# Kernel tuning notes

Measured on AMD Instinct MI355X. Metric: run time of the kernel, lower is better.

Reference implementation:

```python
import jax, jax.numpy as jnp
import numpy as np

K_ACT = 5          # k_active regimes
TAU = 0.5          # resample temperature
N = 8192           # n_particles (scaled to production size)
DZ, DM, KT, DE = 32, 64, 15, 16  # d_latent, d_mamba, k_regimes+10, d_regime_embed


def _lin(x, W, b):
    # torch nn.Linear convention: y = x @ W.T + b
    return x @ W.T + b


def setup_inputs() -> dict:
    key = jax.random.key(0)
    ks = iter(jax.random.split(key, 48))

    def rn(shape, s=1.0):
        return jax.random.normal(next(ks), shape, jnp.float32) * s

    inp = dict(
        remaining_high=jax.random.uniform(next(ks), (N,), jnp.float32) * 5.0 + 1.0,
        remaining_low=jax.random.uniform(next(ks), (N,), jnp.float32) * 5.0 + 1.0,
        z=rn((N, DZ)),
        regime_logits=rn((N, KT)),
        log_weights=rn((N,), 0.5),
        h_t=rn((DM,)),
        obs_remaining=jnp.float32(3.0),
        eps_high=rn((N,)),
        eps_low=rn((N,)),
        u_gumbel=jax.random.uniform(next(ks), (N, N), jnp.float32),
        embed=rn((KT, DE), 0.1),
        W_rt1=rn((32, DM + DE), 0.1), b_rt1=jnp.zeros(32, jnp.float32),
        W_rt2=rn((KT, 32), 0.1), b_rt2=jnp.zeros(KT, jnp.float32),
        W_d1=rn((64, DM + DE + DZ), 0.1), b_d1=jnp.zeros(64, jnp.float32),
        W_d2=rn((32, 64), 0.1), b_d2=jnp.zeros(32, jnp.float32),
        W_d3=rn((4, 32), 0.1), b_d3=jnp.zeros(4, jnp.float32),
        W_g=rn((DZ, DM + DE + DZ), 0.1), b_g=jnp.zeros(DZ, jnp.float32),
        W_c=rn((DZ, DM + DE + DZ), 0.1), b_c=jnp.zeros(DZ, jnp.float32),
        log_R=jnp.array([np.log(0.5), np.log(0.4), np.log(0.6)], jnp.float32),
        log_obs_scale=rn((KT,), 0.1),
        W_a1=rn((16, DM), 0.1), b_a1=jnp.zeros(16, jnp.float32),
        W_a2=rn((1, 16), 0.1), b_a2=jnp.zeros(1, jnp.float32),
    )
    return inp


def reference(remaining_high, remaining_low, z, regime_logits, log_weights, h_t,
              obs_remaining, eps_high, eps_low, u_gumbel, embed,
              W_rt1, b_rt1, W_rt2, b_rt2, W_d1, b_d1, W_d2, b_d2, W_d3, b_d3,
              W_g, b_g, W_c, b_c, log_R, log_obs_scale, W_a1, b_a1, W_a2, b_a2):
    silu = jax.nn.silu
    n = remaining_high.shape[0]
    h = jnp.broadcast_to(h_t, (n, h_t.shape[0]))  # (N, d_mamba)

    # ---- transition (predict step) ----
    rp = jax.nn.softmax(regime_logits, axis=-1)[:, :K_ACT]          # (N, K)
    remb = rp @ embed[:K_ACT]                                        # (N, d_embed)
    ri = jnp.concatenate([h, remb], axis=-1)                         # (N, 80)
    upd = _lin(silu(_lin(ri, W_rt1, b_rt1)), W_rt2, b_rt2)[:, :K_ACT]
    new_logits = regime_logits.at[:, :K_ACT].set(
        0.7 * regime_logits[:, :K_ACT] + 0.3 * upd)
    di = jnp.concatenate([h, remb, z], axis=-1)                      # (N, 112)
    dp = _lin(silu(_lin(silu(_lin(di, W_d1, b_d1)), W_d2, b_d2)), W_d3, b_d3)
    sig_h = jax.nn.softplus(dp[:, 2]) + 0.01
    sig_l = jax.nn.softplus(dp[:, 3]) + 0.01
    nh = jnp.clip(remaining_high + dp[:, 0] + sig_h * eps_high, 0.0)
    nl = jnp.clip(remaining_low + dp[:, 1] + sig_l * eps_low, 0.0)
    gate = jax.nn.sigmoid(_lin(di, W_g, b_g))
    nz = gate * z + (1.0 - gate) * jnp.tanh(_lin(di, W_c, b_c))

    # ---- observation: skew-normal log-likelihood (source_idx=0, 'high') ----
    R_src = jnp.clip(jnp.exp(log_R[0]), 0.15, 2.5)
    alpha = _lin(silu(_lin(h_t[None, :], W_a1, b_a1)), W_a2, b_a2)[0, 0]
    scales = jax.nn.softplus(log_obs_scale[:K_ACT])
    nrp = jax.nn.softmax(new_logits, axis=-1)[:, :K_ACT]
    R = jnp.clip(R_src * (nrp @ scales), 0.15, 4.0)                  # (N,)
    zz = (obs_remaining - nh) / R
    loglik = (jnp.log(2.0) - jnp.log(R) - 0.5 * jnp.log(2.0 * jnp.pi)
              - 0.5 * zz * zz + jax.scipy.stats.norm.logcdf(alpha * zz))

    # ---- weight update + normalization ----
    lw = log_weights + loglik
    lw = lw - jax.scipy.special.logsumexp(lw)

    # ---- soft resample (Gumbel-softmax relaxation) ----
    g = -jnp.log(-jnp.log(u_gumbel + 1e-10) + 1e-10)                 # (N, N)
    sa = jax.nn.softmax((lw[None, :] + g) / TAU, axis=-1)            # (N, N)
    state = jnp.concatenate([nh[:, None], nl[:, None], nz, new_logits], axis=-1)  # (N, 49)
    return sa @ state  # resampled [high | low | z | regime_logits]
```

## Files before the change

### kernel.cpp

```cpp
#include <hip/hip_runtime.h>
#include <math.h>

#define NP 8192

using f32x4  = __attribute__((ext_vector_type(4))) float;
using bf16x4 = __attribute__((ext_vector_type(4))) short;
using bf16x8 = __attribute__((ext_vector_type(8))) short;

__device__ __forceinline__ unsigned short f2bf(float x) {
  unsigned int u = __float_as_uint(x);
  u = (u + 0x7FFFu + ((u >> 16) & 1u)) >> 16;
  return (unsigned short)u;
}
__device__ __forceinline__ float fast_log2(float x) { float r; asm("v_log_f32 %0, %1" : "=v"(r) : "v"(x)); return r; }
__device__ __forceinline__ float fast_exp2(float x) { float r; asm("v_exp_f32 %0, %1" : "=v"(r) : "v"(x)); return r; }
__device__ __forceinline__ float siluf(float x) { return x / (1.0f + expf(-x)); }
__device__ __forceinline__ float softplusf(float x) { return (x > 20.0f) ? x : log1pf(expf(x)); }
__device__ __forceinline__ float dot4(const float4 a, const float4 b) {
  return a.x * b.x + a.y * b.y + a.z * b.z + a.w * b.w;
}


__global__ __launch_bounds__(128) void k_particle(
    const float* __restrict__ rh,   const float* __restrict__ rlo,
    const float* __restrict__ z,    const float* __restrict__ rlog,
    const float* __restrict__ logw, const float* __restrict__ h_t,
    const float* __restrict__ obs_p,
    const float* __restrict__ eps_h, const float* __restrict__ eps_l,
    const float* __restrict__ embed,
    const float* __restrict__ W_rt1, const float* __restrict__ b_rt1,
    const float* __restrict__ W_rt2, const float* __restrict__ b_rt2,
    const float* __restrict__ W_d1,  const float* __restrict__ b_d1,
    const float* __restrict__ W_d2,  const float* __restrict__ b_d2,
    const float* __restrict__ W_d3,  const float* __restrict__ b_d3,
    const float* __restrict__ W_g,   const float* __restrict__ b_g,
    const float* __restrict__ W_c,   const float* __restrict__ b_c,
    const float* __restrict__ log_R, const float* __restrict__ log_obs_scale,
    const float* __restrict__ W_a1,  const float* __restrict__ b_a1,
    const float* __restrict__ W_a2,  const float* __restrict__ b_a2,
    float* __restrict__ a_out, unsigned short* __restrict__ Bt) {
  __shared__ float d1c[64 * 48];
  __shared__ float gcs[32 * 48];
  __shared__ float ccs[32 * 48];
  __shared__ float rt1c[32 * 16];
  __shared__ float d2s[32 * 64];
  __shared__ float d3s[4 * 32];
  __shared__ float rt2s[5 * 32];
  __shared__ float embs[80];
  __shared__ float cD1[64], cRT1[32], cG[32], cC[32];
  __shared__ float bD2[32], bD3[4], bRT2[8];
  __shared__ float a1s[16], scal[8];
  __shared__ float x1ex[32 * 68];
  __shared__ float tx[32 * 36];
  __shared__ float stex[32 * 52];

  const int t = threadIdx.x;

#define STAGEM(DST, SRC, ROWS, SSTR, C0, NC)                          \
  for (int e = t; e < (ROWS) * (NC); e += 128) {                      \
    const int ro = e / (NC);                                          \
    const int co = e - ro * (NC);                                     \
    DST[e] = SRC[ro * (SSTR) + (C0) + co];                            \
  }
  STAGEM(d1c, W_d1, 64, 112, 64, 48)
  STAGEM(gcs, W_g, 32, 112, 64, 48)
  STAGEM(ccs, W_c, 32, 112, 64, 48)
  STAGEM(rt1c, W_rt1, 32, 80, 64, 16)
#undef STAGEM
  for (int e = t; e < 2048; e += 128) d2s[e] = W_d2[e];
  if (t < 128) d3s[t] = W_d3[t];
  for (int e = t; e < 160; e += 128) rt2s[e] = W_rt2[e];
  if (t < 80) embs[t] = embed[t];
  if (t < 32) bD2[t] = b_d2[t];
  if (t < 4)  bD3[t] = b_d3[t];
  if (t < 5)  bRT2[t] = b_rt2[t];

  for (int o = t; o < 160; o += 128) {
    const float* wr; float bb;
    if (o < 64)       { wr = W_d1 + o * 112;        bb = b_d1[o]; }
    else if (o < 96)  { wr = W_rt1 + (o - 64) * 80; bb = b_rt1[o - 64]; }
    else if (o < 128) { wr = W_g + (o - 96) * 112;  bb = b_g[o - 96]; }
    else              { wr = W_c + (o - 128) * 112; bb = b_c[o - 128]; }
    float acc = bb;
    #pragma unroll
    for (int m = 0; m < 64; m += 4)
      acc += dot4(*(const float4*)(wr + m), *(const float4*)(h_t + m));
    if (o < 64) cD1[o] = acc;
    else if (o < 96) cRT1[o - 64] = acc;
    else if (o < 128) cG[o - 96] = acc;
    else cC[o - 128] = acc;
  }
  if (t < 16) {
    float acc = b_a1[t];
    #pragma unroll
    for (int m = 0; m < 64; m += 4)
      acc += dot4(*(const float4*)(W_a1 + t * 64 + m), *(const float4*)(h_t + m));
    a1s[t] = siluf(acc);
  } else if (t == 16) {
    scal[1] = fminf(fmaxf(expf(log_R[0]), 0.15f), 2.5f);
  } else if (t >= 17 && t < 22) {
    scal[2 + t - 17] = softplusf(log_obs_scale[t - 17]);
  }
  __syncthreads();
  if (t == 0) {
    float acc = b_a2[0];
    #pragma unroll
    for (int k = 0; k < 16; ++k) acc += W_a2[k] * a1s[k];
    scal[0] = acc;
  }

  const int l = t & 63, lbase = l & ~3;
  const int q = t >> 2, s = t & 3;
  const int j = blockIdx.x * 32 + q;
  const float obs = obs_p[0];

  float rlj[15];
  #pragma unroll
  for (int k = 0; k < 15; ++k) rlj[k] = rlog[j * 15 + k];
  float m0 = rlj[0];
  #pragma unroll
  for (int k = 1; k < 15; ++k) m0 = fmaxf(m0, rlj[k]);
  float sum = 0.0f, e5[5];
  #pragma unroll
  for (int k = 0; k < 15; ++k) { float e = expf(rlj[k] - m0); if (k < 5) e5[k] = e; sum += e; }
  const float inv = 1.0f / sum;

  float remb[16];
  #pragma unroll
  for (int c = 0; c < 16; ++c) {
    float acc = e5[0] * embs[c];
    #pragma unroll
    for (int k = 1; k < 5; ++k) acc += e5[k] * embs[k * 16 + c];
    remb[c] = acc * inv;
  }

  float zj[32];
  #pragma unroll
  for (int c = 0; c < 32; c += 4) {
    const float4 v = *(const float4*)(z + j * 32 + c);
    zj[c] = v.x; zj[c + 1] = v.y; zj[c + 2] = v.z; zj[c + 3] = v.w;
  }

  #pragma unroll
  for (int r = 0; r < 8; ++r) {
    const int o = 4 * r + s;
    float acc = cRT1[o];
    #pragma unroll
    for (int c = 0; c < 16; ++c) acc += rt1c[o * 16 + c] * remb[c];
    tx[q * 36 + o] = siluf(acc);
  }
  __syncthreads();
  float t1[32];
  #pragma unroll
  for (int c = 0; c < 32; c += 4) {
    const float4 v = *(const float4*)(tx + q * 36 + c);
    t1[c] = v.x; t1[c + 1] = v.y; t1[c + 2] = v.z; t1[c + 3] = v.w;
  }
  float updS = bRT2[s], upd4 = bRT2[4];
  #pragma unroll
  for (int c = 0; c < 32; ++c) { updS += rt2s[s * 32 + c] * t1[c]; upd4 += rt2s[128 + c] * t1[c]; }
  float nlg[15];
  #pragma unroll
  for (int k = 0; k < 4; ++k) nlg[k] = 0.7f * rlj[k] + 0.3f * __shfl(updS, lbase + k);
  nlg[4] = 0.7f * rlj[4] + 0.3f * upd4;
  #pragma unroll
  for (int k = 5; k < 15; ++k) nlg[k] = rlj[k];

  #pragma unroll
  for (int r = 0; r < 16; ++r) {
    const int o = 4 * r + s;
    const float* wrow = d1c + o * 48;
    float acc = cD1[o];
    #pragma unroll
    for (int c = 0; c < 16; ++c) acc += wrow[c] * remb[c];
    #pragma unroll
    for (int c = 0; c < 32; ++c) acc += wrow[16 + c] * zj[c];
    x1ex[q * 68 + o] = siluf(acc);
  }
  __syncthreads();

  float acc8[8];
  #pragma unroll
  for (int r = 0; r < 8; ++r) acc8[r] = bD2[4 * r + s];
  #pragma unroll
  for (int half = 0; half < 2; ++half) {
    float xh[32];
    #pragma unroll
    for (int c = 0; c < 32; c += 4) {
      const float4 v = *(const float4*)(x1ex + q * 68 + half * 32 + c);
      xh[c] = v.x; xh[c + 1] = v.y; xh[c + 2] = v.z; xh[c + 3] = v.w;
    }
    #pragma unroll
    for (int r = 0; r < 8; ++r) {
      const int o = 4 * r + s;
      #pragma unroll
      for (int c = 0; c < 32; ++c) acc8[r] += d2s[o * 64 + half * 32 + c] * xh[c];
    }
  }
  #pragma unroll
  for (int r = 0; r < 8; ++r) tx[q * 36 + 4 * r + s] = siluf(acc8[r]);
  __syncthreads();
  float x2v[32];
  #pragma unroll
  for (int c = 0; c < 32; c += 4) {
    const float4 v = *(const float4*)(tx + q * 36 + c);
    x2v[c] = v.x; x2v[c + 1] = v.y; x2v[c + 2] = v.z; x2v[c + 3] = v.w;
  }
  float dps = bD3[s];
  #pragma unroll
  for (int c = 0; c < 32; ++c) dps += d3s[s * 32 + c] * x2v[c];
  const float dp0 = __shfl(dps, lbase), dp1 = __shfl(dps, lbase + 1);
  const float dp2 = __shfl(dps, lbase + 2), dp3 = __shfl(dps, lbase + 3);
  const float sig_h = softplusf(dp2) + 0.01f;
  const float sig_l = softplusf(dp3) + 0.01f;
  const float nh = fmaxf(rh[j] + dp0 + sig_h * eps_h[j], 0.0f);
  const float nl = fmaxf(rlo[j] + dp1 + sig_l * eps_l[j], 0.0f);

  #pragma unroll
  for (int r = 0; r < 8; ++r) {
    const int o = 4 * r + s;
    const float* gr = gcs + o * 48;
    const float* cr = ccs + o * 48;
    float ga = cG[o], caa = cC[o];
    #pragma unroll
    for (int c = 0; c < 16; ++c) { ga += gr[c] * remb[c]; caa += cr[c] * remb[c]; }
    #pragma unroll
    for (int c = 0; c < 32; ++c) { ga += gr[16 + c] * zj[c]; caa += cr[16 + c] * zj[c]; }
    const float gs = 1.0f / (1.0f + expf(-ga));
    stex[q * 52 + 2 + o] = gs * zj[o] + (1.0f - gs) * tanhf(caa);
  }

  if (s == 0) {
    stex[q * 52 + 0] = nh;
    stex[q * 52 + 1] = nl;
    #pragma unroll
    for (int k = 0; k < 15; ++k) stex[q * 52 + 34 + k] = nlg[k];
    float m1 = nlg[0];
    #pragma unroll
    for (int k = 1; k < 15; ++k) m1 = fmaxf(m1, nlg[k]);
    float sum1 = 0.0f, e5b[5];
    #pragma unroll
    for (int k = 0; k < 15; ++k) { float e = expf(nlg[k] - m1); if (k < 5) e5b[k] = e; sum1 += e; }
    float dot = 0.0f;
    #pragma unroll
    for (int k = 0; k < 5; ++k) dot += e5b[k] * scal[2 + k];
    dot /= sum1;
    const float R  = fminf(fmaxf(scal[1] * dot, 0.15f), 4.0f);
    const float zz = (obs - nh) / R;
    const float xx = scal[0] * zz;
    float lcdf;
    if (xx > -6.0f) {
      double p = 0.5 * erfc(-(double)xx * 0.7071067811865475244);
      lcdf = (float)log(p);
    } else {
      const float ix2 = 1.0f / (xx * xx);
      const float ser = 1.0f + ix2 * (-1.0f + ix2 * (3.0f + ix2 * (-15.0f + ix2 * 105.0f)));
      lcdf = -0.5f * xx * xx - logf(-xx) - 0.918938533f + logf(ser);
    }
    const float loglik = 0.693147181f - logf(R) - 0.918938533f - 0.5f * zz * zz + lcdf;
    a_out[j] = (logw[j] + loglik) * 2.8853900817779268f;
  }
  __syncthreads();

  if (t < 64) {
    const int c = t;
    const int b = c >> 4, rowc = c & 15;
    if (c < 49) {
      #pragma unroll
      for (int m = 0; m < 4; ++m) {
        bf16x8 v8;
        #pragma unroll
        for (int r = 0; r < 8; ++r) v8[r] = (short)f2bf(stex[(8 * m + r) * 52 + c]);
        *(bf16x8*)(Bt + (size_t)(((blockIdx.x * 4 + b) * 64) + m * 16 + rowc) * 8) = v8;
      }
    } else if (c == 49) {
      bf16x8 v8;
      #pragma unroll
      for (int r = 0; r < 8; ++r) v8[r] = (short)0x3F80;
      #pragma unroll
      for (int m = 0; m < 4; ++m)
        *(bf16x8*)(Bt + (size_t)(((blockIdx.x * 4 + b) * 64) + m * 16 + rowc) * 8) = v8;
    } else {
      bf16x8 v8;
      #pragma unroll
      for (int r = 0; r < 8; ++r) v8[r] = 0;
      #pragma unroll
      for (int m = 0; m < 4; ++m)
        *(bf16x8*)(Bt + (size_t)(((blockIdx.x * 4 + b) * 64) + m * 16 + rowc) * 8) = v8;
    }
  }
}

#define RSTR 136
__global__ __launch_bounds__(512) void k_resample(const float* __restrict__ u,
                                                  const float* __restrict__ a,
                                                  const unsigned short* __restrict__ Bt,
                                                  float* __restrict__ out) {
  __shared__ unsigned short Wlds[8][16][RSTR];
  __shared__ float cacc[8][64][16];
  __shared__ float zrow[16];
  const int t = threadIdx.x;
  const int w = t >> 6, l = t & 63;
  const int i0 = blockIdx.x << 4;
  const int jw = w << 10;
  const int lc = (l & 31) << 2;
  const int rh2 = l >> 5;

  f32x4 acc0 = {0.f, 0.f, 0.f, 0.f}, acc1 = acc0, acc2 = acc0, acc3 = acc0;

  for (int g = 0; g < 8; ++g) {
    const int cb = jw + (g << 7);
    const float4 av = *(const float4*)(a + cb + lc);
    float4 uv[8];
    #pragma unroll
    for (int q2 = 0; q2 < 8; ++q2) {
      const int row = (q2 << 1) + rh2;
      uv[q2] = *(const float4*)(u + (size_t)(i0 + row) * NP + cb + lc);
    }
    #pragma unroll
    for (int q2 = 0; q2 < 8; ++q2) {
      const int row = (q2 << 1) + rh2;
      bf16x4 wv4;
      #pragma unroll
      for (int e = 0; e < 4; ++e) {
        const float ue = (e == 0) ? uv[q2].x : (e == 1) ? uv[q2].y : (e == 2) ? uv[q2].z : uv[q2].w;
        const float ae = (e == 0) ? av.x : (e == 1) ? av.y : (e == 2) ? av.z : av.w;
        const float t1 = fast_log2(ue + 1e-10f);
        const float t2 = fmaf(t1, -0.69314718056f, 1e-10f);
        const float t3 = fast_log2(t2);
        wv4[e] = (short)f2bf(fast_exp2(fmaf(t3, -2.0f, ae)));
      }
      *(bf16x4*)(&Wlds[w][row][lc]) = wv4;
    }
    #pragma unroll
    for (int kbl = 0; kbl < 4; ++kbl) {
      const int jblk = (cb >> 5) + kbl;
      const bf16x8 af = *(const bf16x8*)(&Wlds[w][l & 15][(kbl << 5) + ((l >> 4) << 3)]);
      const unsigned short* bp = Bt + (size_t)(jblk << 2) * 512;
      const bf16x8 b0 = *(const bf16x8*)(bp + (0 * 64 + l) * 8);
      const bf16x8 b1 = *(const bf16x8*)(bp + (1 * 64 + l) * 8);
      const bf16x8 b2 = *(const bf16x8*)(bp + (2 * 64 + l) * 8);
      const bf16x8 b3 = *(const bf16x8*)(bp + (3 * 64 + l) * 8);
      acc0 = __builtin_amdgcn_mfma_f32_16x16x32_bf16(af, b0, acc0, 0, 0, 0);
      acc1 = __builtin_amdgcn_mfma_f32_16x16x32_bf16(af, b1, acc1, 0, 0, 0);
      acc2 = __builtin_amdgcn_mfma_f32_16x16x32_bf16(af, b2, acc2, 0, 0, 0);
      acc3 = __builtin_amdgcn_mfma_f32_16x16x32_bf16(af, b3, acc3, 0, 0, 0);
    }
  }

  __syncthreads();
  #pragma unroll
  for (int r = 0; r < 4; ++r) {
    cacc[w][l][0 * 4 + r] = acc0[r];
    cacc[w][l][1 * 4 + r] = acc1[r];
    cacc[w][l][2 * 4 + r] = acc2[r];
    cacc[w][l][3 * 4 + r] = acc3[r];
  }
  __syncthreads();

  const int c = t & 63;
  float v[2];
  #pragma unroll
  for (int rr = 0; rr < 2; ++rr) {
    const int r    = ((t >> 6) << 1) + rr;
    const int lsrc = ((r >> 2) << 4) | (c & 15);
    const int reg  = ((c >> 4) << 2) + (r & 3);
    float sv = 0.0f;
    #pragma unroll
    for (int ww = 0; ww < 8; ++ww) sv += cacc[ww][lsrc][reg];
    v[rr] = sv;
    if (c == 49) zrow[r] = sv;
  }
  __syncthreads();
  if (c < 49) {
    #pragma unroll
    for (int rr = 0; rr < 2; ++rr) {
      const int r = ((t >> 6) << 1) + rr;
      out[(size_t)(i0 + r) * 49 + c] = v[rr] / zrow[r];
    }
  }
}

extern "C" void kernel_launch(void* const* d_in, const int* in_sizes, int n_in,
                              void* d_out, int out_size, void* d_ws, size_t ws_size,
                              hipStream_t stream) {
  const float* rh    = (const float*)d_in[0];
  const float* rlo   = (const float*)d_in[1];
  const float* z     = (const float*)d_in[2];
  const float* rlog  = (const float*)d_in[3];
  const float* logw  = (const float*)d_in[4];
  const float* h_t   = (const float*)d_in[5];
  const float* obs   = (const float*)d_in[6];
  const float* eps_h = (const float*)d_in[7];
  const float* eps_l = (const float*)d_in[8];
  const float* u     = (const float*)d_in[9];
  const float* embed = (const float*)d_in[10];
  const float* W_rt1 = (const float*)d_in[11];
  const float* b_rt1 = (const float*)d_in[12];
  const float* W_rt2 = (const float*)d_in[13];
  const float* b_rt2 = (const float*)d_in[14];
  const float* W_d1  = (const float*)d_in[15];
  const float* b_d1  = (const float*)d_in[16];
  const float* W_d2  = (const float*)d_in[17];
  const float* b_d2  = (const float*)d_in[18];
  const float* W_d3  = (const float*)d_in[19];
  const float* b_d3  = (const float*)d_in[20];
  const float* W_g   = (const float*)d_in[21];
  const float* b_g   = (const float*)d_in[22];
  const float* W_c   = (const float*)d_in[23];
  const float* b_c   = (const float*)d_in[24];
  const float* log_R = (const float*)d_in[25];
  const float* log_obs_scale = (const float*)d_in[26];
  const float* W_a1  = (const float*)d_in[27];
  const float* b_a1  = (const float*)d_in[28];
  const float* W_a2  = (const float*)d_in[29];
  const float* b_a2  = (const float*)d_in[30];

  float* ws_a = (float*)((char*)d_ws + 36864);
  unsigned short* ws_bt = (unsigned short*)((char*)d_ws + 73728);

  k_particle<<<256, 128, 0, stream>>>(rh, rlo, z, rlog, logw, h_t, obs, eps_h, eps_l,
                                      embed, W_rt1, b_rt1, W_rt2, b_rt2,
                                      W_d1, b_d1, W_d2, b_d2, W_d3, b_d3,
                                      W_g, b_g, W_c, b_c, log_R, log_obs_scale,
                                      W_a1, b_a1, W_a2, b_a2, ws_a, ws_bt);
  k_resample<<<512, 512, 0, stream>>>(u, ws_a, ws_bt, (float*)d_out);
}
```

Measured before the change: 470.6 us.

## Double-buffer Gumbel tile loads, widen groups, and replace log/exp with reciprocal

The resample kernel now processes 256-column groups per wave and software-pipelines the global loads of the uniform noise tile: the next group's 16 rows are prefetched into registers while the current group is transformed and fed to MFMA. The Gumbel weight exp(a - 2*log(-log u)) is rewritten algebraically as exp2(a) * rcp(X)^2, replacing one log and one per-element exp with a reciprocal and hoisting exp2(a) out of the row loop. The LDS staging buffer and the cross-wave reduction buffer are aliased into one shared array. The cost is much higher register use from two 16-float4 tiles, which may lower occupancy or cause spills.

```diff
diff --git a/kernel.cpp b/kernel.cpp
--- a/kernel.cpp
+++ b/kernel.cpp
@@ -2,6 +2,7 @@
 #include <math.h>
 
 #define NP 8192
+#define RSTR 264
 
 using f32x4  = __attribute__((ext_vector_type(4))) float;
 using bf16x4 = __attribute__((ext_vector_type(4))) short;
@@ -14,6 +15,7 @@
 }
 __device__ __forceinline__ float fast_log2(float x) { float r; asm("v_log_f32 %0, %1" : "=v"(r) : "v"(x)); return r; }
 __device__ __forceinline__ float fast_exp2(float x) { float r; asm("v_exp_f32 %0, %1" : "=v"(r) : "v"(x)); return r; }
+__device__ __forceinline__ float fast_rcp(float x)  { float r; asm("v_rcp_f32 %0, %1" : "=v"(r) : "v"(x)); return r; }
 __device__ __forceinline__ float siluf(float x) { return x / (1.0f + expf(-x)); }
 __device__ __forceinline__ float softplusf(float x) { return (x > 20.0f) ? x : log1pf(expf(x)); }
 __device__ __forceinline__ float dot4(const float4 a, const float4 b) {
@@ -291,51 +293,81 @@
   }
 }
 
-#define RSTR 136
+struct UTile { float4 v[16]; };
+
+__device__ __forceinline__ void load_group(UTile& ut, float4& av,
+                                           const float* __restrict__ u,
+                                           const float* __restrict__ a,
+                                           int i0, int cb, int lc4) {
+  #pragma unroll
+  for (int r = 0; r < 16; ++r)
+    ut.v[r] = *(const float4*)(u + (size_t)(i0 + r) * NP + cb + lc4);
+  av = *(const float4*)(a + cb + lc4);
+}
+
+__device__ __forceinline__ void transform_store(const UTile& ut, const float4 av,
+                                                unsigned short* __restrict__ Wwave, int lc4) {
+  const float e2a0 = fast_exp2(av.x), e2a1 = fast_exp2(av.y);
+  const float e2a2 = fast_exp2(av.z), e2a3 = fast_exp2(av.w);
+  #pragma unroll
+  for (int r = 0; r < 16; ++r) {
+    bf16x4 o;
+    const float xs0 = ut.v[r].x, xs1 = ut.v[r].y, xs2 = ut.v[r].z, xs3 = ut.v[r].w;
+    {
+      const float X = fmaf(fast_log2(xs0 + 1e-10f), -0.69314718056f, 1e-10f);
+      const float rr = fast_rcp(X);
+      o[0] = (short)f2bf(e2a0 * rr * rr);
+    }
+    {
+      const float X = fmaf(fast_log2(xs1 + 1e-10f), -0.69314718056f, 1e-10f);
+      const float rr = fast_rcp(X);
+      o[1] = (short)f2bf(e2a1 * rr * rr);
+    }
+    {
+      const float X = fmaf(fast_log2(xs2 + 1e-10f), -0.69314718056f, 1e-10f);
+      const float rr = fast_rcp(X);
+      o[2] = (short)f2bf(e2a2 * rr * rr);
+    }
+    {
+      const float X = fmaf(fast_log2(xs3 + 1e-10f), -0.69314718056f, 1e-10f);
+      const float rr = fast_rcp(X);
+      o[3] = (short)f2bf(e2a3 * rr * rr);
+    }
+    *(bf16x4*)(Wwave + r * RSTR + lc4) = o;
+  }
+}
+
 __global__ __launch_bounds__(512) void k_resample(const float* __restrict__ u,
                                                   const float* __restrict__ a,
                                                   const unsigned short* __restrict__ Bt,
                                                   float* __restrict__ out) {
-  __shared__ unsigned short Wlds[8][16][RSTR];
-  __shared__ float cacc[8][64][16];
+  __shared__ __align__(16) char smem[8 * 16 * RSTR * 2];
   __shared__ float zrow[16];
   const int t = threadIdx.x;
   const int w = t >> 6, l = t & 63;
   const int i0 = blockIdx.x << 4;
   const int jw = w << 10;
-  const int lc = (l & 31) << 2;
-  const int rh2 = l >> 5;
+  const int lc4 = l << 2;
+  unsigned short* Wwave = (unsigned short*)smem + w * 16 * RSTR;
 
   f32x4 acc0 = {0.f, 0.f, 0.f, 0.f}, acc1 = acc0, acc2 = acc0, acc3 = acc0;
 
-  for (int g = 0; g < 8; ++g) {
-    const int cb = jw + (g << 7);
-    const float4 av = *(const float4*)(a + cb + lc);
-    float4 uv[8];
-    #pragma unroll
-    for (int q2 = 0; q2 < 8; ++q2) {
-      const int row = (q2 << 1) + rh2;
-      uv[q2] = *(const float4*)(u + (size_t)(i0 + row) * NP + cb + lc);
-    }
-    #pragma unroll
-    for (int q2 = 0; q2 < 8; ++q2) {
-      const int row = (q2 << 1) + rh2;
-      bf16x4 wv4;
-      #pragma unroll
-      for (int e = 0; e < 4; ++e) {
-        const float ue = (e == 0) ? uv[q2].x : (e == 1) ? uv[q2].y : (e == 2) ? uv[q2].z : uv[q2].w;
-        const float ae = (e == 0) ? av.x : (e == 1) ? av.y : (e == 2) ? av.z : av.w;
-        const float t1 = fast_log2(ue + 1e-10f);
-        const float t2 = fmaf(t1, -0.69314718056f, 1e-10f);
-        const float t3 = fast_log2(t2);
-        wv4[e] = (short)f2bf(fast_exp2(fmaf(t3, -2.0f, ae)));
-      }
-      *(bf16x4*)(&Wlds[w][row][lc]) = wv4;
-    }
-    #pragma unroll
-    for (int kbl = 0; kbl < 4; ++kbl) {
-      const int jblk = (cb >> 5) + kbl;
-      const bf16x8 af = *(const bf16x8*)(&Wlds[w][l & 15][(kbl << 5) + ((l >> 4) << 3)]);
+  UTile tA, tB; float4 aA, aB;
+  load_group(tA, aA, u, a, i0, jw, lc4);
+
+  #pragma unroll
+  for (int g = 0; g < 4; ++g) {
+    const int cb = jw + (g << 8);
+    if (g < 3) {
+      if (g & 1) load_group(tA, aA, u, a, i0, cb + 256, lc4);
+      else       load_group(tB, aB, u, a, i0, cb + 256, lc4);
+    }
+    if (g & 1) transform_store(tB, aB, Wwave, lc4);
+    else       transform_store(tA, aA, Wwave, lc4);
+    #pragma unroll
+    for (int kbl = 0; kbl < 8; ++kbl) {
+      const bf16x8 af = *(const bf16x8*)(Wwave + (l & 15) * RSTR + (kbl << 5) + ((l >> 4) << 3));
+      const int jblk = (jw >> 5) + (g << 3) + kbl;
       const unsigned short* bp = Bt + (size_t)(jblk << 2) * 512;
       const bf16x8 b0 = *(const bf16x8*)(bp + (0 * 64 + l) * 8);
       const bf16x8 b1 = *(const bf16x8*)(bp + (1 * 64 + l) * 8);
@@ -349,12 +381,14 @@
   }
 
   __syncthreads();
+  float* cacc = (float*)smem;
+  float* crow = cacc + (w * 64 + l) * 16;
   #pragma unroll
   for (int r = 0; r < 4; ++r) {
-    cacc[w][l][0 * 4 + r] = acc0[r];
-    cacc[w][l][1 * 4 + r] = acc1[r];
-    cacc[w][l][2 * 4 + r] = acc2[r];
-    cacc[w][l][3 * 4 + r] = acc3[r];
+    crow[0 * 4 + r] = acc0[r];
+    crow[1 * 4 + r] = acc1[r];
+    crow[2 * 4 + r] = acc2[r];
+    crow[3 * 4 + r] = acc3[r];
   }
   __syncthreads();
 
@@ -367,7 +401,7 @@
     const int reg  = ((c >> 4) << 2) + (r & 3);
     float sv = 0.0f;
     #pragma unroll
-    for (int ww = 0; ww < 8; ++ww) sv += cacc[ww][lsrc][reg];
+    for (int ww = 0; ww < 8; ++ww) sv += cacc[(ww * 64 + lsrc) * 16 + reg];
     v[rr] = sv;
     if (c == 49) zrow[r] = sv;
   }
```

Measured after the change: 544.2 us. 15.6% more time.

## Double-buffer Gumbel tiles in resample kernel and simplify weight transform

Applied to the files above, without the earlier changes.

The resample kernel now processes 64-column tiles with two LDS buffers per wave. The next tile's global loads are issued and transformed while MFMAs run on the current tile, so memory latency overlaps with matrix work. The Gumbel weight exp(a - 2*log(-log u)) is rewritten as exp2(a)/X^2 using a reciprocal instead of a second log and exp per element. The accumulator staging buffer now reuses the tile LDS, cutting shared memory per block, though the rcp-based form may differ numerically near edge cases.

```diff
diff --git a/kernel.cpp b/kernel.cpp
--- a/kernel.cpp
+++ b/kernel.cpp
@@ -2,6 +2,8 @@
 #include <math.h>
 
 #define NP 8192
+#define TSTR 72
+#define TILE_ELE (16 * TSTR)
 
 using f32x4  = __attribute__((ext_vector_type(4))) float;
 using bf16x4 = __attribute__((ext_vector_type(4))) short;
@@ -14,6 +16,7 @@
 }
 __device__ __forceinline__ float fast_log2(float x) { float r; asm("v_log_f32 %0, %1" : "=v"(r) : "v"(x)); return r; }
 __device__ __forceinline__ float fast_exp2(float x) { float r; asm("v_exp_f32 %0, %1" : "=v"(r) : "v"(x)); return r; }
+__device__ __forceinline__ float fast_rcp(float x)  { float r; asm("v_rcp_f32 %0, %1" : "=v"(r) : "v"(x)); return r; }
 __device__ __forceinline__ float siluf(float x) { return x / (1.0f + expf(-x)); }
 __device__ __forceinline__ float softplusf(float x) { return (x > 20.0f) ? x : log1pf(expf(x)); }
 __device__ __forceinline__ float dot4(const float4 a, const float4 b) {
@@ -291,70 +294,100 @@
   }
 }
 
-#define RSTR 136
+struct Quad { float4 q0, q1, q2, q3, av; };
+
+__device__ __forceinline__ void load_tile(Quad& Q, const float* __restrict__ u,
+                                          const float* __restrict__ a,
+                                          int i0, int cb, int r0, int c0) {
+  Q.q0 = *(const float4*)(u + (size_t)(i0 + r0 + 0)  * NP + cb + c0);
+  Q.q1 = *(const float4*)(u + (size_t)(i0 + r0 + 4)  * NP + cb + c0);
+  Q.q2 = *(const float4*)(u + (size_t)(i0 + r0 + 8)  * NP + cb + c0);
+  Q.q3 = *(const float4*)(u + (size_t)(i0 + r0 + 12) * NP + cb + c0);
+  Q.av = *(const float4*)(a + cb + c0);
+}
+
+__device__ __forceinline__ void xform4(const float4 uv, const float4 e2a, unsigned short* dst) {
+  bf16x4 o;
+  { const float X = fmaf(fast_log2(uv.x + 1e-10f), -0.69314718056f, 1e-10f);
+    const float r = fast_rcp(X); o[0] = (short)f2bf(e2a.x * r * r); }
+  { const float X = fmaf(fast_log2(uv.y + 1e-10f), -0.69314718056f, 1e-10f);
+    const float r = fast_rcp(X); o[1] = (short)f2bf(e2a.y * r * r); }
+  { const float X = fmaf(fast_log2(uv.z + 1e-10f), -0.69314718056f, 1e-10f);
+    const float r = fast_rcp(X); o[2] = (short)f2bf(e2a.z * r * r); }
+  { const float X = fmaf(fast_log2(uv.w + 1e-10f), -0.69314718056f, 1e-10f);
+    const float r = fast_rcp(X); o[3] = (short)f2bf(e2a.w * r * r); }
+  *(bf16x4*)dst = o;
+}
+
+__device__ __forceinline__ void xform_tile(const Quad& Q, unsigned short* tp, int r0, int c0) {
+  float4 e2a;
+  e2a.x = fast_exp2(Q.av.x); e2a.y = fast_exp2(Q.av.y);
+  e2a.z = fast_exp2(Q.av.z); e2a.w = fast_exp2(Q.av.w);
+  xform4(Q.q0, e2a, tp + (r0 + 0)  * TSTR + c0);
+  xform4(Q.q1, e2a, tp + (r0 + 4)  * TSTR + c0);
+  xform4(Q.q2, e2a, tp + (r0 + 8)  * TSTR + c0);
+  xform4(Q.q3, e2a, tp + (r0 + 12) * TSTR + c0);
+}
+
+__device__ __forceinline__ void mfma_tile(f32x4& a0, f32x4& a1, f32x4& a2, f32x4& a3,
+                                          const unsigned short* tp,
+                                          const unsigned short* __restrict__ Bt,
+                                          int jblk0, int l) {
+  #pragma unroll
+  for (int kb = 0; kb < 2; ++kb) {
+    const bf16x8 af = *(const bf16x8*)(tp + (l & 15) * TSTR + (kb << 5) + ((l >> 4) << 3));
+    const unsigned short* bp = Bt + (size_t)((jblk0 + kb) << 2) * 512;
+    const bf16x8 b0 = *(const bf16x8*)(bp + (0 * 64 + l) * 8);
+    const bf16x8 b1 = *(const bf16x8*)(bp + (1 * 64 + l) * 8);
+    const bf16x8 b2 = *(const bf16x8*)(bp + (2 * 64 + l) * 8);
+    const bf16x8 b3 = *(const bf16x8*)(bp + (3 * 64 + l) * 8);
+    a0 = __builtin_amdgcn_mfma_f32_16x16x32_bf16(af, b0, a0, 0, 0, 0);
+    a1 = __builtin_amdgcn_mfma_f32_16x16x32_bf16(af, b1, a1, 0, 0, 0);
+    a2 = __builtin_amdgcn_mfma_f32_16x16x32_bf16(af, b2, a2, 0, 0, 0);
+    a3 = __builtin_amdgcn_mfma_f32_16x16x32_bf16(af, b3, a3, 0, 0, 0);
+  }
+}
+
 __global__ __launch_bounds__(512) void k_resample(const float* __restrict__ u,
                                                   const float* __restrict__ a,
                                                   const unsigned short* __restrict__ Bt,
                                                   float* __restrict__ out) {
-  __shared__ unsigned short Wlds[8][16][RSTR];
-  __shared__ float cacc[8][64][16];
+  __shared__ __align__(16) unsigned short tiles[8 * 2 * TILE_ELE];
   __shared__ float zrow[16];
   const int t = threadIdx.x;
   const int w = t >> 6, l = t & 63;
   const int i0 = blockIdx.x << 4;
   const int jw = w << 10;
-  const int lc = (l & 31) << 2;
-  const int rh2 = l >> 5;
+  const int r0 = l >> 4;
+  const int c0 = (l & 15) << 2;
+  unsigned short* tw = tiles + w * 2 * TILE_ELE;
 
   f32x4 acc0 = {0.f, 0.f, 0.f, 0.f}, acc1 = acc0, acc2 = acc0, acc3 = acc0;
 
-  for (int g = 0; g < 8; ++g) {
-    const int cb = jw + (g << 7);
-    const float4 av = *(const float4*)(a + cb + lc);
-    float4 uv[8];
-    #pragma unroll
-    for (int q2 = 0; q2 < 8; ++q2) {
-      const int row = (q2 << 1) + rh2;
-      uv[q2] = *(const float4*)(u + (size_t)(i0 + row) * NP + cb + lc);
-    }
-    #pragma unroll
-    for (int q2 = 0; q2 < 8; ++q2) {
-      const int row = (q2 << 1) + rh2;
-      bf16x4 wv4;
-      #pragma unroll
-      for (int e = 0; e < 4; ++e) {
-        const float ue = (e == 0) ? uv[q2].x : (e == 1) ? uv[q2].y : (e == 2) ? uv[q2].z : uv[q2].w;
-        const float ae = (e == 0) ? av.x : (e == 1) ? av.y : (e == 2) ? av.z : av.w;
-        const float t1 = fast_log2(ue + 1e-10f);
-        const float t2 = fmaf(t1, -0.69314718056f, 1e-10f);
-        const float t3 = fast_log2(t2);
-        wv4[e] = (short)f2bf(fast_exp2(fmaf(t3, -2.0f, ae)));
-      }
-      *(bf16x4*)(&Wlds[w][row][lc]) = wv4;
-    }
-    #pragma unroll
-    for (int kbl = 0; kbl < 4; ++kbl) {
-      const int jblk = (cb >> 5) + kbl;
-      const bf16x8 af = *(const bf16x8*)(&Wlds[w][l & 15][(kbl << 5) + ((l >> 4) << 3)]);
-      const unsigned short* bp = Bt + (size_t)(jblk << 2) * 512;
-      const bf16x8 b0 = *(const bf16x8*)(bp + (0 * 64 + l) * 8);
-      const bf16x8 b1 = *(const bf16x8*)(bp + (1 * 64 + l) * 8);
-      const bf16x8 b2 = *(const bf16x8*)(bp + (2 * 64 + l) * 8);
-      const bf16x8 b3 = *(const bf16x8*)(bp + (3 * 64 + l) * 8);
-      acc0 = __builtin_amdgcn_mfma_f32_16x16x32_bf16(af, b0, acc0, 0, 0, 0);
-      acc1 = __builtin_amdgcn_mfma_f32_16x16x32_bf16(af, b1, acc1, 0, 0, 0);
-      acc2 = __builtin_amdgcn_mfma_f32_16x16x32_bf16(af, b2, acc2, 0, 0, 0);
-      acc3 = __builtin_amdgcn_mfma_f32_16x16x32_bf16(af, b3, acc3, 0, 0, 0);
-    }
-  }
-
-  __syncthreads();
+  Quad QA, QB;
+  load_tile(QA, u, a, i0, jw, r0, c0);
+  xform_tile(QA, tw, r0, c0);
+
+  #pragma unroll
+  for (int gp = 0; gp < 8; ++gp) {
+    const int g0 = gp * 2;
+    load_tile(QB, u, a, i0, jw + (g0 + 1) * 64, r0, c0);
+    mfma_tile(acc0, acc1, acc2, acc3, tw, Bt, (jw + g0 * 64) >> 5, l);
+    xform_tile(QB, tw + TILE_ELE, r0, c0);
+    if (gp < 7) load_tile(QA, u, a, i0, jw + (g0 + 2) * 64, r0, c0);
+    mfma_tile(acc0, acc1, acc2, acc3, tw + TILE_ELE, Bt, (jw + (g0 + 1) * 64) >> 5, l);
+    if (gp < 7) xform_tile(QA, tw, r0, c0);
+  }
+
+  __syncthreads();
+  float* cacc = (float*)tiles;
+  float* crow = cacc + (w * 64 + l) * 16;
   #pragma unroll
   for (int r = 0; r < 4; ++r) {
-    cacc[w][l][0 * 4 + r] = acc0[r];
-    cacc[w][l][1 * 4 + r] = acc1[r];
-    cacc[w][l][2 * 4 + r] = acc2[r];
-    cacc[w][l][3 * 4 + r] = acc3[r];
+    crow[0 * 4 + r] = acc0[r];
+    crow[1 * 4 + r] = acc1[r];
+    crow[2 * 4 + r] = acc2[r];
+    crow[3 * 4 + r] = acc3[r];
   }
   __syncthreads();
 
@@ -367,7 +400,7 @@
     const int reg  = ((c >> 4) << 2) + (r & 3);
     float sv = 0.0f;
     #pragma unroll
-    for (int ww = 0; ww < 8; ++ww) sv += cacc[ww][lsrc][reg];
+    for (int ww = 0; ww < 8; ++ww) sv += cacc[(ww * 64 + lsrc) * 16 + reg];
     v[rr] = sv;
     if (c == 49) zrow[r] = sv;
   }
```

New measurement: 477.9 us. No clear change (+1.5%).
